# Optimization experiments

Measured on AMD Instinct MI355X. Metric: run time of the kernel, lower is better.

Reference implementation:

```python
import jax, jax.numpy as jnp
import numpy as np

B, M, E, R, U, I = 4096, 100, 128, 64, 100000, 100000


def setup_inputs() -> dict:
    key = jax.random.key(0)
    ks = jax.random.split(key, 10)
    return {
        "user_id": jax.random.randint(ks[0], (B,), 0, U),
        "item_id_p": jax.random.randint(ks[1], (B,), 0, I),
        "item_id_n": jax.random.randint(ks[2], (B,), 0, I),
        "inter_id": jax.random.randint(ks[3], (B, M), 0, I),
        "user_emb_w": jax.random.normal(ks[4], (U, E), jnp.float32),
        "item_emb_w": jax.random.normal(ks[5], (I, E), jnp.float32),
        "ua_key": jax.random.normal(ks[6], (R, E), jnp.float32),
        "ua_val": jax.random.normal(ks[7], (R, E), jnp.float32),
        "ia_key": jax.random.normal(ks[8], (R, E), jnp.float32),
        "ia_val": jax.random.normal(ks[9], (R, E), jnp.float32),
    }


def _maxnorm_lookup(w, ids, max_norm=1.0, eps=1e-7):
    # torch nn.Embedding(max_norm=1): rows with norm > max_norm are renormalized
    v = w[ids]
    n = jnp.linalg.norm(v, axis=-1, keepdims=True)
    scale = jnp.where(n > max_norm, max_norm / (n + eps), jnp.ones_like(n))
    return v * scale


def _rel_attn(key_w, val_w, mul_feat, attn_feat, inter):
    # w = key*val elementwise (R,E); einsum 'mbj,ij->bmj' sums w over relations
    wsum = jnp.sum(key_w * val_w, axis=0)                 # (E,)
    rel = mul_feat[:, None, :] * inter * wsum             # (B,M,E) rel_vecs
    logits = jnp.einsum("bme,be->bm", rel, attn_feat)      # (B,M)
    attn = jax.nn.softmax(logits, axis=1)
    return jnp.einsum("bm,bme->be", attn, rel)             # (B,E)


def reference(user_id, item_id_p, item_id_n, inter_id,
              user_emb_w, item_emb_w, ua_key, ua_val, ia_key, ia_val):
    u = _maxnorm_lookup(user_emb_w, user_id)
    ip = _maxnorm_lookup(item_emb_w, item_id_p)
    inn = _maxnorm_lookup(item_emb_w, item_id_n)
    inter = _maxnorm_lookup(item_emb_w, inter_id)
    # UserAttention: rel from item*inter, softmax vs user
    # ItemAttention (model_type='plus'): rel from user*inter, softmax vs item
    rel_p = _rel_attn(ua_key, ua_val, ip, u, inter) + _rel_attn(ia_key, ia_val, u, ip, inter)
    rel_n = _rel_attn(ua_key, ua_val, inn, u, inter) + _rel_attn(ia_key, ia_val, u, inn, inter)
    return (u, ip, inn, rel_p, rel_n)
```

## Files before the change

### kernel.cpp

```cpp
#include <hip/hip_runtime.h>
#include <math.h>

#define BB 4096
#define MM 100
#define EE 128
#define RR 64

__device__ __forceinline__ float4 ld4(const float* p) {
    return *reinterpret_cast<const float4*>(p);
}
__device__ __forceinline__ void st4(float* p, float4 v) {
    *reinterpret_cast<float4*>(p) = v;
}
__device__ __forceinline__ float f4dot(float4 a, float4 b) {
    return a.x * b.x + a.y * b.y + a.z * b.z + a.w * b.w;
}
__device__ __forceinline__ float4 f4mul3(float4 a, float4 b, float4 c) {
    float4 r;
    r.x = a.x * b.x * c.x; r.y = a.y * b.y * c.y;
    r.z = a.z * b.z * c.z; r.w = a.w * b.w * c.w;
    return r;
}
__device__ __forceinline__ float4 f4fma(float4 v, float s, float4 acc) {
    acc.x += v.x * s; acc.y += v.y * s; acc.z += v.z * s; acc.w += v.w * s;
    return acc;
}
__device__ __forceinline__ float4 f4red(float4 a, int off) {
    a.x += __shfl_xor(a.x, off, 64); a.y += __shfl_xor(a.y, off, 64);
    a.z += __shfl_xor(a.z, off, 64); a.w += __shfl_xor(a.w, off, 64);
    return a;
}

template<int CTRL>
__device__ __forceinline__ float dpp_add(float x) {
    int y = __builtin_amdgcn_update_dpp(0, __float_as_int(x), CTRL, 0xF, 0xF, true);
    return x + __int_as_float(y);
}
__device__ __forceinline__ float row16_allreduce(float x) {
    x = dpp_add<0x121>(x);
    x = dpp_add<0x122>(x);
    x = dpp_add<0x124>(x);
    x = dpp_add<0x128>(x);
    return x;
}

__global__ __launch_bounds__(512)
void wsum_kernel(const float* __restrict__ ua_key, const float* __restrict__ ua_val,
                 const float* __restrict__ ia_key, const float* __restrict__ ia_val,
                 float* __restrict__ ws) {
    __shared__ float part[4][EE];
    const float* k = (blockIdx.x == 0) ? ua_key : ia_key;
    const float* v = (blockIdx.x == 0) ? ua_val : ia_val;
    int e = threadIdx.x & 127;
    int q = threadIdx.x >> 7;
    float s = 0.f;
    #pragma unroll
    for (int j = 0; j < 16; ++j) {
        int r = q * 16 + j;
        s += k[r * EE + e] * v[r * EE + e];
    }
    part[q][e] = s;
    __syncthreads();
    if (threadIdx.x < EE)
        ws[blockIdx.x * EE + e] = part[0][e] + part[1][e] + part[2][e] + part[3][e];
}

__global__ __launch_bounds__(256)
void hlrm_main(const int* __restrict__ user_id,
               const int* __restrict__ ip_id,
               const int* __restrict__ in_id,
               const int* __restrict__ inter_id,
               const float* __restrict__ user_w,
               const float* __restrict__ item_w,
               const float* __restrict__ ws,
               float* __restrict__ out) {
    __shared__ float s_u[EE], s_ip[EE], s_in[EE];
    __shared__ float s_part[4][4][EE];
    __shared__ float s_den[4][4];

    const int b    = blockIdx.x;
    const int tid  = threadIdx.x;
    const int lane = tid & 63;
    const int wave = tid >> 6;
    const int g    = lane >> 4;
    const int hl   = lane & 15;
    const int wg   = wave * 4 + g;
    const int e0   = hl * 4;
    const int e1   = 64 + hl * 4;

    int idreg = 0;
    if (lane < 28) {
        int row = (lane >> 2) * 16 + wave * 4 + (lane & 3);
        if (row < MM) idreg = inter_id[b * MM + row];
    }
    int ids[7];
    #pragma unroll
    for (int i = 0; i < 7; ++i) ids[i] = __shfl(idreg, i * 4 + g);

    float4 va0, vb0, va1, vb1, va2, vb2;
    {
        uint o = (uint)ids[0] * EE; va0 = ld4(item_w + o + e0); vb0 = ld4(item_w + o + e1);
        o = (uint)ids[1] * EE;      va1 = ld4(item_w + o + e0); vb1 = ld4(item_w + o + e1);
        o = (uint)ids[2] * EE;      va2 = ld4(item_w + o + e0); vb2 = ld4(item_w + o + e1);
    }

    if (wave == 0 || (wave == 1 && lane < 32)) {
        const int half32 = lane >> 5, l32 = lane & 31;
        const float* src; int id; float* dst;
        if (wave == 0 && half32 == 0) { id = user_id[b]; src = user_w; dst = s_u;  }
        else if (wave == 0)           { id = ip_id[b];   src = item_w; dst = s_ip; }
        else                          { id = in_id[b];   src = item_w; dst = s_in; }
        float4 v = ld4(src + (size_t)id * EE + l32 * 4);
        float ss = f4dot(v, v);
        #pragma unroll
        for (int off = 1; off < 32; off <<= 1) ss += __shfl_xor(ss, off, 64);
        float n  = sqrtf(ss);
        float sc = (n > 1.f) ? 1.f / (n + 1e-7f) : 1.f;
        float4 o; o.x = v.x * sc; o.y = v.y * sc; o.z = v.z * sc; o.w = v.w * sc;
        st4(dst + l32 * 4, o);
    }
    __syncthreads();

    float4 ua  = ld4(s_u + e0),  ub  = ld4(s_u + e1);
    float4 pa  = ld4(s_ip + e0), pb  = ld4(s_ip + e1);
    float4 ia  = ld4(s_in + e0), ib  = ld4(s_in + e1);
    float4 waa = ld4(ws + e0),   wab = ld4(ws + e1);
    float4 wia = ld4(ws + EE + e0), wib = ld4(ws + EE + e1);
    float4 qa0 = f4mul3(ua, pa, waa), qb0 = f4mul3(ub, pb, wab);
    float4 qa1 = f4mul3(ua, pa, wia), qb1 = f4mul3(ub, pb, wib);
    float4 qa2 = f4mul3(ua, ia, waa), qb2 = f4mul3(ub, ib, wab);
    float4 qa3 = f4mul3(ua, ia, wia), qb3 = f4mul3(ub, ib, wib);

    if (tid < EE) {
        size_t base = (size_t)b * EE + tid;
        out[0 * (size_t)BB * EE + base] = s_u[tid];
        out[1 * (size_t)BB * EE + base] = s_ip[tid];
        out[2 * (size_t)BB * EE + base] = s_in[tid];
    }

    float4 Sa0 = {0,0,0,0}, Sa1 = {0,0,0,0}, Sa2 = {0,0,0,0}, Sa3 = {0,0,0,0};
    float4 Sb0 = {0,0,0,0}, Sb1 = {0,0,0,0}, Sb2 = {0,0,0,0}, Sb3 = {0,0,0,0};
    float den0 = 0.f, den1 = 0.f, den2 = 0.f, den3 = 0.f;

#define LOADT(VA, VB, I) do {                                  \
        uint o = (uint)ids[I] * EE;                            \
        VA = ld4(item_w + o + e0);                             \
        VB = ld4(item_w + o + e1);                             \
    } while (0)

#define STEP(VA, VB, I) do {                                                   \
        float ss = f4dot(VA, VA)  + f4dot(VB, VB);                             \
        float d0 = f4dot(VA, qa0) + f4dot(VB, qb0);                            \
        float d1 = f4dot(VA, qa1) + f4dot(VB, qb1);                            \
        float d2 = f4dot(VA, qa2) + f4dot(VB, qb2);                            \
        float d3 = f4dot(VA, qa3) + f4dot(VB, qb3);                            \
        ss = row16_allreduce(ss);                                              \
        d0 = row16_allreduce(d0); d1 = row16_allreduce(d1);                    \
        d2 = row16_allreduce(d2); d3 = row16_allreduce(d3);                    \
        float sc = (ss > 1.f) ? __builtin_amdgcn_rsqf(ss) : 1.f;               \
        float w0 = __expf(d0 * sc), w1 = __expf(d1 * sc);                      \
        float w2 = __expf(d2 * sc), w3 = __expf(d3 * sc);                      \
        if ((I) == 6 && wg >= 4) { w0 = 0.f; w1 = 0.f; w2 = 0.f; w3 = 0.f; }   \
        den0 += w0; den1 += w1; den2 += w2; den3 += w3;                        \
        w0 *= sc; w1 *= sc; w2 *= sc; w3 *= sc;                                \
        Sa0 = f4fma(VA, w0, Sa0); Sb0 = f4fma(VB, w0, Sb0);                    \
        Sa1 = f4fma(VA, w1, Sa1); Sb1 = f4fma(VB, w1, Sb1);                    \
        Sa2 = f4fma(VA, w2, Sa2); Sb2 = f4fma(VB, w2, Sb2);                    \
        Sa3 = f4fma(VA, w3, Sa3); Sb3 = f4fma(VB, w3, Sb3);                    \
    } while (0)

    STEP(va0, vb0, 0); LOADT(va0, vb0, 3);
    STEP(va1, vb1, 1); LOADT(va1, vb1, 4);
    STEP(va2, vb2, 2); LOADT(va2, vb2, 5);
    STEP(va0, vb0, 3); LOADT(va0, vb0, 6);
    STEP(va1, vb1, 4);
    STEP(va2, vb2, 5);
    STEP(va0, vb0, 6);

#undef STEP
#undef LOADT

    #pragma unroll
    for (int off = 16; off < 64; off <<= 1) {
        Sa0 = f4red(Sa0, off); Sb0 = f4red(Sb0, off);
        Sa1 = f4red(Sa1, off); Sb1 = f4red(Sb1, off);
        Sa2 = f4red(Sa2, off); Sb2 = f4red(Sb2, off);
        Sa3 = f4red(Sa3, off); Sb3 = f4red(Sb3, off);
        den0 += __shfl_xor(den0, off, 64);
        den1 += __shfl_xor(den1, off, 64);
        den2 += __shfl_xor(den2, off, 64);
        den3 += __shfl_xor(den3, off, 64);
    }
    if (g == 0) {
        st4(&s_part[wave][0][e0], Sa0); st4(&s_part[wave][0][e1], Sb0);
        st4(&s_part[wave][1][e0], Sa1); st4(&s_part[wave][1][e1], Sb1);
        st4(&s_part[wave][2][e0], Sa2); st4(&s_part[wave][2][e1], Sb2);
        st4(&s_part[wave][3][e0], Sa3); st4(&s_part[wave][3][e1], Sb3);
        if (hl == 0) {
            s_den[wave][0] = den0; s_den[wave][1] = den1;
            s_den[wave][2] = den2; s_den[wave][3] = den3;
        }
    }
    __syncthreads();

    if (tid < EE) {
        int e = tid;
        float D0 = s_den[0][0] + s_den[1][0] + s_den[2][0] + s_den[3][0];
        float D1 = s_den[0][1] + s_den[1][1] + s_den[2][1] + s_den[3][1];
        float D2 = s_den[0][2] + s_den[1][2] + s_den[2][2] + s_den[3][2];
        float D3 = s_den[0][3] + s_den[1][3] + s_den[2][3] + s_den[3][3];
        float S0e = (s_part[0][0][e] + s_part[1][0][e] + s_part[2][0][e] + s_part[3][0][e]) / D0;
        float S1e = (s_part[0][1][e] + s_part[1][1][e] + s_part[2][1][e] + s_part[3][1][e]) / D1;
        float S2e = (s_part[0][2][e] + s_part[1][2][e] + s_part[2][2][e] + s_part[3][2][e]) / D2;
        float S3e = (s_part[0][3][e] + s_part[1][3][e] + s_part[2][3][e] + s_part[3][3][e]) / D3;
        float u = s_u[e], ip = s_ip[e], inn = s_in[e];
        float wae = ws[e], wie = ws[EE + e];
        float relp = ip  * wae * S0e + u * wie * S1e;
        float reln = inn * wae * S2e + u * wie * S3e;
        size_t base = (size_t)b * EE + e;
        out[3 * (size_t)BB * EE + base] = relp;
        out[4 * (size_t)BB * EE + base] = reln;
    }
}

extern "C" void kernel_launch(void* const* d_in, const int* in_sizes, int n_in,
                              void* d_out, int out_size, void* d_ws, size_t ws_size,
                              hipStream_t stream) {
    const int*   user_id   = (const int*)d_in[0];
    const int*   item_id_p = (const int*)d_in[1];
    const int*   item_id_n = (const int*)d_in[2];
    const int*   inter_id  = (const int*)d_in[3];
    const float* user_w    = (const float*)d_in[4];
    const float* item_w    = (const float*)d_in[5];
    const float* ua_key    = (const float*)d_in[6];
    const float* ua_val    = (const float*)d_in[7];
    const float* ia_key    = (const float*)d_in[8];
    const float* ia_val    = (const float*)d_in[9];
    float* out = (float*)d_out;
    float* ws  = (float*)d_ws;

    wsum_kernel<<<2, 512, 0, stream>>>(ua_key, ua_val, ia_key, ia_val, ws);
    hlrm_main<<<BB, 256, 0, stream>>>(user_id, item_id_p, item_id_n, inter_id,
                                      user_w, item_w, ws, out);
}
```

Before: 50.45 us.

## Map one batch row per wave instead of per block, drop LDS reductions

Each wave now handles a whole batch row (4 rows per block, BB/4 blocks), staging its 100 interaction ids in LDS and looping over 25 rows per quarter-wave with a 5-deep register prefetch. The user/pos/neg rows are normalized in-wave by folding the max-norm scale into the query vectors. The cross-wave shared-memory partial reduction and both __syncthreads barriers go away, and the output stores are spread across the four 16-lane groups as float4 writes. In exchange each wave runs a longer serial loop with less memory parallelism per row, and the user/item rows are reloaded at the end.

```diff
diff --git a/kernel.cpp b/kernel.cpp
--- a/kernel.cpp
+++ b/kernel.cpp
@@ -21,6 +21,10 @@
     r.z = a.z * b.z * c.z; r.w = a.w * b.w * c.w;
     return r;
 }
+__device__ __forceinline__ float4 f4scale(float4 a, float s) {
+    float4 r; r.x = a.x * s; r.y = a.y * s; r.z = a.z * s; r.w = a.w * s;
+    return r;
+}
 __device__ __forceinline__ float4 f4fma(float4 v, float s, float4 acc) {
     acc.x += v.x * s; acc.y += v.y * s; acc.z += v.z * s; acc.w += v.w * s;
     return acc;
@@ -29,6 +33,15 @@
     a.x += __shfl_xor(a.x, off, 64); a.y += __shfl_xor(a.y, off, 64);
     a.z += __shfl_xor(a.z, off, 64); a.w += __shfl_xor(a.w, off, 64);
     return a;
+}
+__device__ __forceinline__ float4 relcomb(float4 x1, float4 w1, float4 S1v, float i1,
+                                          float4 x2, float4 w2, float4 S2v, float i2) {
+    float4 r;
+    r.x = x1.x * w1.x * (S1v.x * i1) + x2.x * w2.x * (S2v.x * i2);
+    r.y = x1.y * w1.y * (S1v.y * i1) + x2.y * w2.y * (S2v.y * i2);
+    r.z = x1.z * w1.z * (S1v.z * i1) + x2.z * w2.z * (S2v.z * i2);
+    r.w = x1.w * w1.w * (S1v.w * i1) + x2.w * w2.w * (S2v.w * i2);
+    return r;
 }
 
 template<int CTRL>
@@ -74,109 +87,102 @@
                const float* __restrict__ item_w,
                const float* __restrict__ ws,
                float* __restrict__ out) {
-    __shared__ float s_u[EE], s_ip[EE], s_in[EE];
-    __shared__ float s_part[4][4][EE];
-    __shared__ float s_den[4][4];
-
-    const int b    = blockIdx.x;
+    __shared__ int s_ids[4][MM];
+
     const int tid  = threadIdx.x;
     const int lane = tid & 63;
     const int wave = tid >> 6;
+    const int b    = blockIdx.x * 4 + wave;
     const int g    = lane >> 4;
     const int hl   = lane & 15;
-    const int wg   = wave * 4 + g;
     const int e0   = hl * 4;
     const int e1   = 64 + hl * 4;
-
-    int idreg = 0;
-    if (lane < 28) {
-        int row = (lane >> 2) * 16 + wave * 4 + (lane & 3);
-        if (row < MM) idreg = inter_id[b * MM + row];
-    }
-    int ids[7];
-    #pragma unroll
-    for (int i = 0; i < 7; ++i) ids[i] = __shfl(idreg, i * 4 + g);
-
-    float4 va0, vb0, va1, vb1, va2, vb2;
-    {
-        uint o = (uint)ids[0] * EE; va0 = ld4(item_w + o + e0); vb0 = ld4(item_w + o + e1);
-        o = (uint)ids[1] * EE;      va1 = ld4(item_w + o + e0); vb1 = ld4(item_w + o + e1);
-        o = (uint)ids[2] * EE;      va2 = ld4(item_w + o + e0); vb2 = ld4(item_w + o + e1);
-    }
-
-    if (wave == 0 || (wave == 1 && lane < 32)) {
-        const int half32 = lane >> 5, l32 = lane & 31;
-        const float* src; int id; float* dst;
-        if (wave == 0 && half32 == 0) { id = user_id[b]; src = user_w; dst = s_u;  }
-        else if (wave == 0)           { id = ip_id[b];   src = item_w; dst = s_ip; }
-        else                          { id = in_id[b];   src = item_w; dst = s_in; }
-        float4 v = ld4(src + (size_t)id * EE + l32 * 4);
-        float ss = f4dot(v, v);
-        #pragma unroll
-        for (int off = 1; off < 32; off <<= 1) ss += __shfl_xor(ss, off, 64);
-        float n  = sqrtf(ss);
-        float sc = (n > 1.f) ? 1.f / (n + 1e-7f) : 1.f;
-        float4 o; o.x = v.x * sc; o.y = v.y * sc; o.z = v.z * sc; o.w = v.w * sc;
-        st4(dst + l32 * 4, o);
-    }
-    __syncthreads();
-
-    float4 ua  = ld4(s_u + e0),  ub  = ld4(s_u + e1);
-    float4 pa  = ld4(s_ip + e0), pb  = ld4(s_ip + e1);
-    float4 ia  = ld4(s_in + e0), ib  = ld4(s_in + e1);
-    float4 waa = ld4(ws + e0),   wab = ld4(ws + e1);
+    int* sw = s_ids[wave];
+
+    if (lane < 50)
+        *reinterpret_cast<int2*>(sw + 2 * lane) =
+            *reinterpret_cast<const int2*>(inter_id + b * MM + 2 * lane);
+
+    int uid = user_id[b], pid = ip_id[b], nid = in_id[b];
+    float4 ru_a = ld4(user_w + (uint)uid * EE + e0);
+    float4 ru_b = ld4(user_w + (uint)uid * EE + e1);
+    float4 rp_a = ld4(item_w + (uint)pid * EE + e0);
+    float4 rp_b = ld4(item_w + (uint)pid * EE + e1);
+    float4 rn_a = ld4(item_w + (uint)nid * EE + e0);
+    float4 rn_b = ld4(item_w + (uint)nid * EE + e1);
+    float4 waa = ld4(ws + e0),      wab = ld4(ws + e1);
     float4 wia = ld4(ws + EE + e0), wib = ld4(ws + EE + e1);
-    float4 qa0 = f4mul3(ua, pa, waa), qb0 = f4mul3(ub, pb, wab);
-    float4 qa1 = f4mul3(ua, pa, wia), qb1 = f4mul3(ub, pb, wib);
-    float4 qa2 = f4mul3(ua, ia, waa), qb2 = f4mul3(ub, ib, wab);
-    float4 qa3 = f4mul3(ua, ia, wia), qb3 = f4mul3(ub, ib, wib);
-
-    if (tid < EE) {
-        size_t base = (size_t)b * EE + tid;
-        out[0 * (size_t)BB * EE + base] = s_u[tid];
-        out[1 * (size_t)BB * EE + base] = s_ip[tid];
-        out[2 * (size_t)BB * EE + base] = s_in[tid];
-    }
+
+    int sid0 = sw[g], sid1 = sw[4 + g], sid2 = sw[8 + g],
+        sid3 = sw[12 + g], sid4 = sw[16 + g];
+    float4 va0, vb0, va1, vb1, va2, vb2, va3, vb3, va4, vb4;
+#define LOADT(J) do {                                   \
+        uint o = (uint)sid##J * EE;                     \
+        va##J = ld4(item_w + o + e0);                   \
+        vb##J = ld4(item_w + o + e1);                   \
+    } while (0)
+    LOADT(0); LOADT(1); LOADT(2); LOADT(3); LOADT(4);
+    sid0 = sw[20 + g]; sid1 = sw[24 + g]; sid2 = sw[28 + g];
+    sid3 = sw[32 + g]; sid4 = sw[36 + g];
+
+    float ssu = f4dot(ru_a, ru_a) + f4dot(ru_b, ru_b);
+    float ssp = f4dot(rp_a, rp_a) + f4dot(rp_b, rp_b);
+    float ssn = f4dot(rn_a, rn_a) + f4dot(rn_b, rn_b);
+    ssu = row16_allreduce(ssu);
+    ssp = row16_allreduce(ssp);
+    ssn = row16_allreduce(ssn);
+    float scu = (ssu > 1.f) ? __builtin_amdgcn_rsqf(ssu) : 1.f;
+    float scp = (ssp > 1.f) ? __builtin_amdgcn_rsqf(ssp) : 1.f;
+    float scn = (ssn > 1.f) ? __builtin_amdgcn_rsqf(ssn) : 1.f;
+
+    float cup = scu * scp, cun = scu * scn;
+    float4 qa0 = f4scale(f4mul3(ru_a, rp_a, waa), cup);
+    float4 qb0 = f4scale(f4mul3(ru_b, rp_b, wab), cup);
+    float4 qa1 = f4scale(f4mul3(ru_a, rp_a, wia), cup);
+    float4 qb1 = f4scale(f4mul3(ru_b, rp_b, wib), cup);
+    float4 qa2 = f4scale(f4mul3(ru_a, rn_a, waa), cun);
+    float4 qb2 = f4scale(f4mul3(ru_b, rn_b, wab), cun);
+    float4 qa3 = f4scale(f4mul3(ru_a, rn_a, wia), cun);
+    float4 qb3 = f4scale(f4mul3(ru_b, rn_b, wib), cun);
 
     float4 Sa0 = {0,0,0,0}, Sa1 = {0,0,0,0}, Sa2 = {0,0,0,0}, Sa3 = {0,0,0,0};
     float4 Sb0 = {0,0,0,0}, Sb1 = {0,0,0,0}, Sb2 = {0,0,0,0}, Sb3 = {0,0,0,0};
     float den0 = 0.f, den1 = 0.f, den2 = 0.f, den3 = 0.f;
 
-#define LOADT(VA, VB, I) do {                                  \
-        uint o = (uint)ids[I] * EE;                            \
-        VA = ld4(item_w + o + e0);                             \
-        VB = ld4(item_w + o + e1);                             \
+#define STEP(J) do {                                                        \
+        float ss = f4dot(va##J, va##J) + f4dot(vb##J, vb##J);               \
+        float d0 = f4dot(va##J, qa0) + f4dot(vb##J, qb0);                   \
+        float d1 = f4dot(va##J, qa1) + f4dot(vb##J, qb1);                   \
+        float d2 = f4dot(va##J, qa2) + f4dot(vb##J, qb2);                   \
+        float d3 = f4dot(va##J, qa3) + f4dot(vb##J, qb3);                   \
+        ss = row16_allreduce(ss);                                           \
+        d0 = row16_allreduce(d0); d1 = row16_allreduce(d1);                 \
+        d2 = row16_allreduce(d2); d3 = row16_allreduce(d3);                 \
+        float sc = (ss > 1.f) ? __builtin_amdgcn_rsqf(ss) : 1.f;            \
+        float w0 = __expf(d0 * sc), w1 = __expf(d1 * sc);                   \
+        float w2 = __expf(d2 * sc), w3 = __expf(d3 * sc);                   \
+        den0 += w0; den1 += w1; den2 += w2; den3 += w3;                     \
+        w0 *= sc; w1 *= sc; w2 *= sc; w3 *= sc;                             \
+        Sa0 = f4fma(va##J, w0, Sa0); Sb0 = f4fma(vb##J, w0, Sb0);           \
+        Sa1 = f4fma(va##J, w1, Sa1); Sb1 = f4fma(vb##J, w1, Sb1);           \
+        Sa2 = f4fma(va##J, w2, Sa2); Sb2 = f4fma(vb##J, w2, Sb2);           \
+        Sa3 = f4fma(va##J, w3, Sa3); Sb3 = f4fma(vb##J, w3, Sb3);           \
     } while (0)
 
-#define STEP(VA, VB, I) do {                                                   \
-        float ss = f4dot(VA, VA)  + f4dot(VB, VB);                             \
-        float d0 = f4dot(VA, qa0) + f4dot(VB, qb0);                            \
-        float d1 = f4dot(VA, qa1) + f4dot(VB, qb1);                            \
-        float d2 = f4dot(VA, qa2) + f4dot(VB, qb2);                            \
-        float d3 = f4dot(VA, qa3) + f4dot(VB, qb3);                            \
-        ss = row16_allreduce(ss);                                              \
-        d0 = row16_allreduce(d0); d1 = row16_allreduce(d1);                    \
-        d2 = row16_allreduce(d2); d3 = row16_allreduce(d3);                    \
-        float sc = (ss > 1.f) ? __builtin_amdgcn_rsqf(ss) : 1.f;               \
-        float w0 = __expf(d0 * sc), w1 = __expf(d1 * sc);                      \
-        float w2 = __expf(d2 * sc), w3 = __expf(d3 * sc);                      \
-        if ((I) == 6 && wg >= 4) { w0 = 0.f; w1 = 0.f; w2 = 0.f; w3 = 0.f; }   \
-        den0 += w0; den1 += w1; den2 += w2; den3 += w3;                        \
-        w0 *= sc; w1 *= sc; w2 *= sc; w3 *= sc;                                \
-        Sa0 = f4fma(VA, w0, Sa0); Sb0 = f4fma(VB, w0, Sb0);                    \
-        Sa1 = f4fma(VA, w1, Sa1); Sb1 = f4fma(VB, w1, Sb1);                    \
-        Sa2 = f4fma(VA, w2, Sa2); Sb2 = f4fma(VB, w2, Sb2);                    \
-        Sa3 = f4fma(VA, w3, Sa3); Sb3 = f4fma(VB, w3, Sb3);                    \
-    } while (0)
-
-    STEP(va0, vb0, 0); LOADT(va0, vb0, 3);
-    STEP(va1, vb1, 1); LOADT(va1, vb1, 4);
-    STEP(va2, vb2, 2); LOADT(va2, vb2, 5);
-    STEP(va0, vb0, 3); LOADT(va0, vb0, 6);
-    STEP(va1, vb1, 4);
-    STEP(va2, vb2, 5);
-    STEP(va0, vb0, 6);
-
+    #pragma unroll 1
+    for (int it = 0; it < 4; ++it) {
+        STEP(0); LOADT(0);
+        STEP(1); LOADT(1);
+        STEP(2); LOADT(2);
+        STEP(3); LOADT(3);
+        STEP(4); LOADT(4);
+        if (it < 3) {
+            int o = (it * 5 + 10) * 4 + g;
+            sid0 = sw[o];      sid1 = sw[o + 4];  sid2 = sw[o + 8];
+            sid3 = sw[o + 12]; sid4 = sw[o + 16];
+        }
+    }
+    STEP(0); STEP(1); STEP(2); STEP(3); STEP(4);
 #undef STEP
 #undef LOADT
 
@@ -191,35 +197,37 @@
         den2 += __shfl_xor(den2, off, 64);
         den3 += __shfl_xor(den3, off, 64);
     }
+    float iD0 = 1.f / den0, iD1 = 1.f / den1, iD2 = 1.f / den2, iD3 = 1.f / den3;
+
+    float4 u_a = f4scale(ld4(user_w + (uint)uid * EE + e0), scu);
+    float4 u_b = f4scale(ld4(user_w + (uint)uid * EE + e1), scu);
+    float4 p_a = f4scale(ld4(item_w + (uint)pid * EE + e0), scp);
+    float4 p_b = f4scale(ld4(item_w + (uint)pid * EE + e1), scp);
+    float4 n_a = f4scale(ld4(item_w + (uint)nid * EE + e0), scn);
+    float4 n_b = f4scale(ld4(item_w + (uint)nid * EE + e1), scn);
+    float4 w0a = ld4(ws + e0),      w0b = ld4(ws + e1);
+    float4 w1a = ld4(ws + EE + e0), w1b = ld4(ws + EE + e1);
+
+    size_t base = (size_t)b * EE;
+    const size_t P = (size_t)BB * EE;
     if (g == 0) {
-        st4(&s_part[wave][0][e0], Sa0); st4(&s_part[wave][0][e1], Sb0);
-        st4(&s_part[wave][1][e0], Sa1); st4(&s_part[wave][1][e1], Sb1);
-        st4(&s_part[wave][2][e0], Sa2); st4(&s_part[wave][2][e1], Sb2);
-        st4(&s_part[wave][3][e0], Sa3); st4(&s_part[wave][3][e1], Sb3);
-        if (hl == 0) {
-            s_den[wave][0] = den0; s_den[wave][1] = den1;
-            s_den[wave][2] = den2; s_den[wave][3] = den3;
-        }
-    }
-    __syncthreads();
-
-    if (tid < EE) {
-        int e = tid;
-        float D0 = s_den[0][0] + s_den[1][0] + s_den[2][0] + s_den[3][0];
-        float D1 = s_den[0][1] + s_den[1][1] + s_den[2][1] + s_den[3][1];
-        float D2 = s_den[0][2] + s_den[1][2] + s_den[2][2] + s_den[3][2];
-        float D3 = s_den[0][3] + s_den[1][3] + s_den[2][3] + s_den[3][3];
-        float S0e = (s_part[0][0][e] + s_part[1][0][e] + s_part[2][0][e] + s_part[3][0][e]) / D0;
-        float S1e = (s_part[0][1][e] + s_part[1][1][e] + s_part[2][1][e] + s_part[3][1][e]) / D1;
-        float S2e = (s_part[0][2][e] + s_part[1][2][e] + s_part[2][2][e] + s_part[3][2][e]) / D2;
-        float S3e = (s_part[0][3][e] + s_part[1][3][e] + s_part[2][3][e] + s_part[3][3][e]) / D3;
-        float u = s_u[e], ip = s_ip[e], inn = s_in[e];
-        float wae = ws[e], wie = ws[EE + e];
-        float relp = ip  * wae * S0e + u * wie * S1e;
-        float reln = inn * wae * S2e + u * wie * S3e;
-        size_t base = (size_t)b * EE + e;
-        out[3 * (size_t)BB * EE + base] = relp;
-        out[4 * (size_t)BB * EE + base] = reln;
+        float4 ra = relcomb(p_a, w0a, Sa0, iD0, u_a, w1a, Sa1, iD1);
+        float4 rb = relcomb(p_b, w0b, Sb0, iD0, u_b, w1b, Sb1, iD1);
+        st4(out + 3 * P + base + e0, ra);
+        st4(out + 3 * P + base + e1, rb);
+    } else if (g == 1) {
+        float4 ra = relcomb(n_a, w0a, Sa2, iD2, u_a, w1a, Sa3, iD3);
+        float4 rb = relcomb(n_b, w0b, Sb2, iD2, u_b, w1b, Sb3, iD3);
+        st4(out + 4 * P + base + e0, ra);
+        st4(out + 4 * P + base + e1, rb);
+    } else if (g == 2) {
+        st4(out + 0 * P + base + e0, u_a);
+        st4(out + 0 * P + base + e1, u_b);
+        st4(out + 1 * P + base + e0, p_a);
+        st4(out + 1 * P + base + e1, p_b);
+    } else {
+        st4(out + 2 * P + base + e0, n_a);
+        st4(out + 2 * P + base + e1, n_b);
     }
 }
 
@@ -240,6 +248,6 @@
     float* ws  = (float*)d_ws;
 
     wsum_kernel<<<2, 512, 0, stream>>>(ua_key, ua_val, ia_key, ia_val, ws);
-    hlrm_main<<<BB, 256, 0, stream>>>(user_id, item_id_p, item_id_n, inter_id,
-                                      user_w, item_w, ws, out);
-}
+    hlrm_main<<<BB / 4, 256, 0, stream>>>(user_id, item_id_p, item_id_n, inter_id,
+                                          user_w, item_w, ws, out);
+}
```

After: 50.39 us. No clear change (-0.1%).
